# Optimization experiments

Measured on AMD Instinct MI355X. Metric: run time of the kernel, lower is better.

Reference implementation:

```python
import jax, jax.numpy as jnp
import numpy as np

# MoEFeedForward from ViziMarketTransformer (h100_moe_preset dims), eval mode (dropout = identity).
D, F, E, K = 512, 2048, 8, 2   # d_model, d_ff, n_experts, top_k
B, T = 8, 4096
AUX_W = 0.01


def setup_inputs() -> dict:
    key = jax.random.key(0)
    k0, k1, k2, k3 = jax.random.split(key, 4)
    s_in = 1.0 / np.sqrt(D)
    s_mid = 1.0 / np.sqrt(F)
    return {
        "x": jax.random.normal(k0, (B, T, D), jnp.float32),
        "router_w": (jax.random.normal(k1, (D, E), jnp.float32) * s_in),   # nn.Linear(d_model, n_experts, bias=False)
        "w1": (jax.random.normal(k2, (E, D, F), jnp.float32) * s_in),      # per-expert Linear(d_model, d_ff)
        "b1": jnp.zeros((E, F), jnp.float32),
        "w2": (jax.random.normal(k3, (E, F, D), jnp.float32) * s_mid),     # per-expert Linear(d_ff, d_model)
        "b2": jnp.zeros((E, D), jnp.float32),
    }


def reference(x, router_w, w1, b1, w2, b2):
    Bb, Tt, Dd = x.shape
    xf = x.reshape(-1, Dd)                                   # (N, D), N = B*T
    logits = xf @ router_w                                   # (N, E)
    topk_vals, topk_idx = jax.lax.top_k(logits, K)           # (N, K)
    topk_w = jax.nn.softmax(topk_vals, axis=-1)              # (N, K)
    # Combine weights per expert: sum over k of softmax weight where topk_idx == e.
    comb = jnp.sum(jax.nn.one_hot(topk_idx, E, dtype=xf.dtype) * topk_w[..., None], axis=1)  # (N, E)
    out = jnp.zeros_like(xf)
    for e in range(E):  # small fixed expert count; tokens fully vectorized
        h = jax.nn.gelu(xf @ w1[e] + b1[e], approximate=False)   # exact GELU, as nn.GELU()
        out = out + comb[:, e:e + 1] * (h @ w2[e] + b2[e])
    # Switch/GShard auxiliary load-balancing loss.
    probs = jax.nn.softmax(logits, axis=-1)
    avg_prob = probs.mean(axis=0)                             # (E,)
    avg_frac = jax.nn.one_hot(topk_idx[:, 0], E, dtype=xf.dtype).mean(axis=0)  # (E,)
    aux_loss = AUX_W * E * jnp.sum(avg_prob * avg_frac)
    return out.reshape(Bb, Tt, Dd), aux_loss
```

## Files before the change

kernel.cpp:

```cpp
#include <hip/hip_runtime.h>
#include <hip/hip_fp16.h>
#include <cstdint>
#include <cstddef>

#define NTOK 32768
#define DM 512
#define FF 2048
#define NE 8
#define BM 128
#define FBLK 128
#define NFB (FF / FBLK)

typedef _Float16 half8 __attribute__((ext_vector_type(8)));
typedef float floatx4 __attribute__((ext_vector_type(4)));

#define LGKM0_BARRIER() do { \
  asm volatile("s_waitcnt lgkmcnt(0)" ::: "memory"); \
  __builtin_amdgcn_s_barrier(); \
} while (0)

__global__ __launch_bounds__(256) void k_transpose(const float* __restrict__ W,
                                                   _Float16* __restrict__ Wt, int R, int C) {
  __shared__ float tile[32][33];
  int e = blockIdx.z;
  int c0 = blockIdx.x * 32, r0 = blockIdx.y * 32;
  const float* Wp = W + (size_t)e * R * C;
  _Float16* Wtp = Wt + (size_t)e * R * C;
  int tx = threadIdx.x & 31, ty = threadIdx.x >> 5;
  #pragma unroll
  for (int rr = ty; rr < 32; rr += 8)
    tile[rr][tx] = Wp[(size_t)(r0 + rr) * C + c0 + tx];
  __syncthreads();
  #pragma unroll
  for (int cc = ty; cc < 32; cc += 8)
    Wtp[(size_t)(c0 + cc) * R + r0 + tx] = (_Float16)tile[tx][cc];
}

__global__ __launch_bounds__(256) void k_router(
    const float* __restrict__ x, const float* __restrict__ rw,
    _Float16* __restrict__ xb, int* __restrict__ route_e, float* __restrict__ route_w,
    int* __restrict__ counts, float* __restrict__ aux_acc) {
  __shared__ float s_p[NE];
  __shared__ float s_c[NE];
  __shared__ int s_cnt[NE];
  int tid = threadIdx.x, lane = tid & 63, wave = tid >> 6;
  if (tid < NE) { s_p[tid] = 0.f; s_c[tid] = 0.f; s_cnt[tid] = 0; }
  __syncthreads();
  int n = blockIdx.x * 4 + wave;
  const float4* xr = (const float4*)(x + (size_t)n * DM + lane * 8);
  float4 x0 = xr[0], x1 = xr[1];
  float xv[8] = {x0.x, x0.y, x0.z, x0.w, x1.x, x1.y, x1.z, x1.w};
  float acc[NE];
  #pragma unroll
  for (int e = 0; e < NE; e++) acc[e] = 0.f;
  const float4* rwv = (const float4*)rw;
  #pragma unroll
  for (int j = 0; j < 8; j++) {
    int d = lane * 8 + j;
    float4 r0 = rwv[d * 2], r1 = rwv[d * 2 + 1];
    float xd = xv[j];
    acc[0] += xd * r0.x; acc[1] += xd * r0.y; acc[2] += xd * r0.z; acc[3] += xd * r0.w;
    acc[4] += xd * r1.x; acc[5] += xd * r1.y; acc[6] += xd * r1.z; acc[7] += xd * r1.w;
  }
  half8 hv;
  #pragma unroll
  for (int j = 0; j < 8; j++) hv[j] = (_Float16)xv[j];
  *(half8*)(xb + (size_t)n * DM + lane * 8) = hv;
  #pragma unroll
  for (int e = 0; e < NE; e++) {
    #pragma unroll
    for (int m = 1; m < 64; m <<= 1) acc[e] += __shfl_xor(acc[e], m);
  }
  if (lane == 0) {
    int e0 = 0; float v0 = acc[0];
    for (int e = 1; e < NE; e++) if (acc[e] > v0) { v0 = acc[e]; e0 = e; }
    int e1 = (e0 == 0) ? 1 : 0; float v1 = acc[e1];
    for (int e = 0; e < NE; e++) if (e != e0 && acc[e] > v1) { v1 = acc[e]; e1 = e; }
    float w0 = 1.f / (1.f + expf(v1 - v0));
    float w1 = 1.f - w0;
    route_e[n] = e0 | (e1 << 8);
    route_w[2 * n] = w0; route_w[2 * n + 1] = w1;
    float mx = acc[0];
    for (int e = 1; e < NE; e++) mx = fmaxf(mx, acc[e]);
    float p[NE]; float s = 0.f;
    for (int e = 0; e < NE; e++) { p[e] = expf(acc[e] - mx); s += p[e]; }
    float inv = 1.f / s;
    atomicAdd(&s_cnt[e0], 1); atomicAdd(&s_cnt[e1], 1);
    for (int e = 0; e < NE; e++) atomicAdd(&s_p[e], p[e] * inv);
    atomicAdd(&s_c[e0], 1.f);
  }
  __syncthreads();
  if (tid < NE) {
    atomicAdd(&counts[tid], s_cnt[tid]);
    atomicAdd(&aux_acc[tid], s_p[tid]);
    atomicAdd(&aux_acc[NE + tid], s_c[tid]);
  }
}

__global__ void k_finalize(const int* __restrict__ counts, int* __restrict__ offsets,
                           int* __restrict__ cursors, const float* __restrict__ aux_acc,
                           float* __restrict__ out_aux) {
  if (threadIdx.x == 0 && blockIdx.x == 0) {
    int off = 0;
    for (int e = 0; e < NE; e++) { offsets[e] = off; cursors[e] = off; off += counts[e]; }
    const float invN = 1.f / (float)NTOK;
    float aux = 0.f;
    for (int e = 0; e < NE; e++) aux += (aux_acc[e] * invN) * (aux_acc[NE + e] * invN);
    out_aux[0] = 0.01f * (float)NE * aux;
  }
}

__global__ __launch_bounds__(256) void k_build(
    const int* __restrict__ route_e, const float* __restrict__ route_w,
    int* __restrict__ cursors, int* __restrict__ tok, float* __restrict__ wgt,
    int* __restrict__ pos) {
  __shared__ int s_cnt[NE];
  __shared__ int s_base[NE];
  int tid = threadIdx.x;
  if (tid < NE) s_cnt[tid] = 0;
  __syncthreads();
  int n = blockIdx.x * 256 + tid;
  int re = route_e[n];
  int e0 = re & 0xff, e1 = (re >> 8) & 0xff;
  float w0 = route_w[2 * n], w1 = route_w[2 * n + 1];
  int p0 = atomicAdd(&s_cnt[e0], 1);
  int p1 = atomicAdd(&s_cnt[e1], 1);
  __syncthreads();
  if (tid < NE) s_base[tid] = atomicAdd(&cursors[tid], s_cnt[tid]);
  __syncthreads();
  int g0 = s_base[e0] + p0, g1 = s_base[e1] + p1;
  tok[g0] = n; wgt[g0] = w0; pos[n] = g0;
  tok[g1] = n; wgt[g1] = w1; pos[NTOK + n] = g1;
}

__global__ __launch_bounds__(512, 2) void k_fused(
    const _Float16* __restrict__ xb, const _Float16* __restrict__ w1t,
    const _Float16* __restrict__ w2t, const float* __restrict__ b1,
    const float* __restrict__ b2, const int* __restrict__ counts,
    const int* __restrict__ offsets, const int* __restrict__ tok,
    const float* __restrict__ wgt, _Float16* __restrict__ yb) {
  int bid = blockIdx.x;
  int e = bid & 7;
  int tm = bid >> 3;
  int cnt = counts[e];
  if (tm * BM >= cnt) return;
  int off = offsets[e];

  __shared__ _Float16 Xs[2][BM * 32];
  __shared__ _Float16 W1s[2][FBLK * 32];
  __shared__ _Float16 Hs[BM * FBLK];
  __shared__ _Float16 W2s[2][DM * 32];

  int tid = threadIdx.x, lane = tid & 63, wave = tid >> 6;
  int wr = wave >> 2, wc = wave & 3;
  int fr = lane & 15, kfi = lane >> 4;
  int swz = (kfi ^ ((fr >> 1) & 3)) * 8;
  int rowL = tid >> 2, kc = (tid & 3) * 8;
  int stw = rowL * 32 + (((tid & 3) ^ ((tid >> 3) & 3)) * 8);
  int rq = (lane >> 4) * 4, cq = lane & 15;

  int tr = tm * BM + rowL;
  int t0 = tok[off + (tr < cnt ? tr : 0)];
  const _Float16* ax = xb + (size_t)t0 * DM + kc;
  const _Float16* w1e = w1t + (size_t)e * FF * DM;
  const _Float16* w2e = w2t + (size_t)e * DM * FF;
  const _Float16* w2p = w2e + (size_t)rowL * FF + kc;

  floatx4 acc[4][8];
  floatx4 zero = {0.f, 0.f, 0.f, 0.f};
  #pragma unroll
  for (int i = 0; i < 4; i++)
    #pragma unroll
    for (int j = 0; j < 8; j++) acc[i][j] = zero;

  #pragma unroll 1
  for (int fb = 0; fb < NFB; fb++) {
    int fbase = fb * FBLK;
    floatx4 acc1[4][2];
    #pragma unroll
    for (int i = 0; i < 4; i++)
      #pragma unroll
      for (int j = 0; j < 2; j++) acc1[i][j] = zero;
    const _Float16* w1p = w1e + (size_t)(fbase + rowL) * DM + kc;
    half8 ra = *(const half8*)(ax);
    half8 rb = *(const half8*)(w1p);
    *(half8*)(&Xs[0][stw]) = ra;
    *(half8*)(&W1s[0][stw]) = rb;
    ra = *(const half8*)(ax + 32);
    rb = *(const half8*)(w1p + 32);
    LGKM0_BARRIER();
    #pragma unroll
    for (int k = 0; k < 16; k++) {
      int cur = k & 1;
      if (k + 1 < 16) {
        *(half8*)(&Xs[cur ^ 1][stw]) = ra;
        *(half8*)(&W1s[cur ^ 1][stw]) = rb;
      }
      if (k + 2 < 16) {
        ra = *(const half8*)(ax + (k + 2) * 32);
        rb = *(const half8*)(w1p + (k + 2) * 32);
      }
      const _Float16* Ab = &Xs[cur][(wr * 64 + fr) * 32 + swz];
      const _Float16* Bb = &W1s[cur][(wc * 32 + fr) * 32 + swz];
      half8 av[4], bv[2];
      #pragma unroll
      for (int i = 0; i < 4; i++) av[i] = *(const half8*)(Ab + i * 512);
      #pragma unroll
      for (int j = 0; j < 2; j++) bv[j] = *(const half8*)(Bb + j * 512);
      __builtin_amdgcn_s_setprio(1);
      #pragma unroll
      for (int i = 0; i < 4; i++)
        #pragma unroll
        for (int j = 0; j < 2; j++)
          acc1[i][j] = __builtin_amdgcn_mfma_f32_16x16x32_f16(av[i], bv[j], acc1[i][j], 0, 0, 0);
      __builtin_amdgcn_s_setprio(0);
      if (k + 1 < 16) LGKM0_BARRIER();
    }
    #pragma unroll
    for (int j = 0; j < 2; j++) {
      int col = wc * 32 + j * 16 + cq;
      float bb = b1[e * FF + fbase + col];
      #pragma unroll
      for (int i = 0; i < 4; i++) {
        #pragma unroll
        for (int r = 0; r < 4; r++) {
          int row = wr * 64 + i * 16 + rq + r;
          float v = acc1[i][j][r] + bb;
          v = 0.5f * v * (1.f + erff(v * 0.70710678118654752f));
          Hs[row * FBLK + (col ^ ((row & 7) << 3))] = (_Float16)v;
        }
      }
    }
    const _Float16* w2q = w2p + fbase;
    half8 rw0 = *(const half8*)(w2q);
    half8 rw1 = *(const half8*)(w2q + (size_t)128 * FF);
    half8 rw2 = *(const half8*)(w2q + (size_t)256 * FF);
    half8 rw3 = *(const half8*)(w2q + (size_t)384 * FF);
    *(half8*)(&W2s[0][stw]) = rw0;
    *(half8*)(&W2s[0][stw + 128 * 32]) = rw1;
    *(half8*)(&W2s[0][stw + 256 * 32]) = rw2;
    *(half8*)(&W2s[0][stw + 384 * 32]) = rw3;
    rw0 = *(const half8*)(w2q + 32);
    rw1 = *(const half8*)(w2q + (size_t)128 * FF + 32);
    rw2 = *(const half8*)(w2q + (size_t)256 * FF + 32);
    rw3 = *(const half8*)(w2q + (size_t)384 * FF + 32);
    LGKM0_BARRIER();
    #pragma unroll
    for (int k = 0; k < 4; k++) {
      int cur = k & 1;
      if (k + 1 < 4) {
        *(half8*)(&W2s[cur ^ 1][stw]) = rw0;
        *(half8*)(&W2s[cur ^ 1][stw + 128 * 32]) = rw1;
        *(half8*)(&W2s[cur ^ 1][stw + 256 * 32]) = rw2;
        *(half8*)(&W2s[cur ^ 1][stw + 384 * 32]) = rw3;
      }
      if (k + 2 < 4) {
        const _Float16* p = w2q + (k + 2) * 32;
        rw0 = *(const half8*)(p);
        rw1 = *(const half8*)(p + (size_t)128 * FF);
        rw2 = *(const half8*)(p + (size_t)256 * FF);
        rw3 = *(const half8*)(p + (size_t)384 * FF);
      }
      half8 av[4], bv[8];
      #pragma unroll
      for (int i = 0; i < 4; i++) {
        int row = wr * 64 + i * 16 + fr;
        int col = k * 32 + kfi * 8;
        av[i] = *(const half8*)(&Hs[row * FBLK + (col ^ ((row & 7) << 3))]);
      }
      const _Float16* Bb2 = &W2s[cur][(wc * 128 + fr) * 32 + swz];
      #pragma unroll
      for (int j = 0; j < 8; j++)
        bv[j] = *(const half8*)(Bb2 + j * 512);
      __builtin_amdgcn_s_setprio(1);
      #pragma unroll
      for (int i = 0; i < 4; i++)
        #pragma unroll
        for (int j = 0; j < 8; j++)
          acc[i][j] = __builtin_amdgcn_mfma_f32_16x16x32_f16(av[i], bv[j], acc[i][j], 0, 0, 0);
      __builtin_amdgcn_s_setprio(0);
      if (k + 1 < 4) LGKM0_BARRIER();
    }
  }
  float bcol[8];
  #pragma unroll
  for (int j = 0; j < 8; j++) bcol[j] = b2[e * DM + wc * 128 + j * 16 + cq];
  #pragma unroll
  for (int i = 0; i < 4; i++) {
    #pragma unroll
    for (int r = 0; r < 4; r++) {
      int row = tm * BM + wr * 64 + i * 16 + rq + r;
      if (row < cnt) {
        float w = wgt[off + row];
        _Float16* yr = yb + (size_t)(off + row) * DM + wc * 128 + cq;
        #pragma unroll
        for (int j = 0; j < 8; j++)
          yr[j * 16] = (_Float16)(w * (acc[i][j][r] + bcol[j]));
      }
    }
  }
}

__global__ __launch_bounds__(256) void k_combine(
    const _Float16* __restrict__ yb, const int* __restrict__ pos,
    float* __restrict__ out) {
  int tid = threadIdx.x, lane = tid & 63, wave = tid >> 6;
  int n = blockIdx.x * 4 + wave;
  int p0 = pos[n], p1 = pos[NTOK + n];
  half8 a = *(const half8*)(yb + (size_t)p0 * DM + lane * 8);
  half8 b = *(const half8*)(yb + (size_t)p1 * DM + lane * 8);
  float4 o0, o1;
  o0.x = (float)a[0] + (float)b[0];
  o0.y = (float)a[1] + (float)b[1];
  o0.z = (float)a[2] + (float)b[2];
  o0.w = (float)a[3] + (float)b[3];
  o1.x = (float)a[4] + (float)b[4];
  o1.y = (float)a[5] + (float)b[5];
  o1.z = (float)a[6] + (float)b[6];
  o1.w = (float)a[7] + (float)b[7];
  float4* op = (float4*)(out + (size_t)n * DM + lane * 8);
  op[0] = o0; op[1] = o1;
}

extern "C" void kernel_launch(void* const* d_in, const int* in_sizes, int n_in,
                              void* d_out, int out_size, void* d_ws, size_t ws_size,
                              hipStream_t stream) {
  const float* x  = (const float*)d_in[0];
  const float* rw = (const float*)d_in[1];
  const float* w1 = (const float*)d_in[2];
  const float* b1 = (const float*)d_in[3];
  const float* w2 = (const float*)d_in[4];
  const float* b2 = (const float*)d_in[5];
  float* out = (float*)d_out;

  uint8_t* ws = (uint8_t*)d_ws;
  _Float16* xb  = (_Float16*)ws;  ws += (size_t)NTOK * DM * 2;
  _Float16* w1t = (_Float16*)ws;  ws += (size_t)NE * FF * DM * 2;
  _Float16* w2t = (_Float16*)ws;  ws += (size_t)NE * DM * FF * 2;
  int*   tok     = (int*)ws;      ws += (size_t)2 * NTOK * 4;
  float* wgt     = (float*)ws;    ws += (size_t)2 * NTOK * 4;
  int*   pos     = (int*)ws;      ws += (size_t)2 * NTOK * 4;
  int*   route_e = (int*)ws;      ws += (size_t)NTOK * 4;
  float* route_w = (float*)ws;    ws += (size_t)NTOK * 8;
  int*   counts  = (int*)ws;      ws += 8 * 4;
  int*   offsets = (int*)ws;      ws += 8 * 4;
  int*   cursors = (int*)ws;      ws += 8 * 4;
  float* aux     = (float*)ws;    ws += 16 * 4;
  _Float16* yb  = (_Float16*)ws;

  hipMemsetAsync(counts, 0, (8 + 8 + 8 + 16) * 4, stream);

  k_transpose<<<dim3(FF / 32, DM / 32, NE), 256, 0, stream>>>(w1, w1t, DM, FF);
  k_transpose<<<dim3(DM / 32, FF / 32, NE), 256, 0, stream>>>(w2, w2t, FF, DM);
  k_router<<<NTOK / 4, 256, 0, stream>>>(x, rw, xb, route_e, route_w, counts, aux);
  k_finalize<<<1, 64, 0, stream>>>(counts, offsets, cursors, aux, out + (size_t)NTOK * DM);
  k_build<<<NTOK / 256, 256, 0, stream>>>(route_e, route_w, cursors, tok, wgt, pos);
  k_fused<<<(NTOK / BM) * NE, 512, 0, stream>>>(
      xb, w1t, w2t, b1, b2, counts, offsets, tok, wgt, yb);
  k_combine<<<NTOK / 4, 256, 0, stream>>>(yb, pos, out);
}
```

Before: 955.6 us.

## Use direct global-to-LDS loads with triple buffering and register-stream W2

```diff
diff --git a/kernel.cpp b/kernel.cpp
--- a/kernel.cpp
+++ b/kernel.cpp
@@ -10,6 +10,7 @@
 #define BM 128
 #define FBLK 128
 #define NFB (FF / FBLK)
+#define XBUF 4096
 
 typedef _Float16 half8 __attribute__((ext_vector_type(8)));
 typedef float floatx4 __attribute__((ext_vector_type(4)));
@@ -18,6 +19,10 @@
   asm volatile("s_waitcnt lgkmcnt(0)" ::: "memory"); \
   __builtin_amdgcn_s_barrier(); \
 } while (0)
+
+#define GLL16(g, l) __builtin_amdgcn_global_load_lds( \
+    (const __attribute__((address_space(1))) uint32_t*)(g), \
+    (__attribute__((address_space(3))) uint32_t*)(l), 16, 0, 0)
 
 __global__ __launch_bounds__(256) void k_transpose(const float* __restrict__ W,
                                                    _Float16* __restrict__ Wt, int R, int C) {
@@ -146,25 +151,25 @@
   if (tm * BM >= cnt) return;
   int off = offsets[e];
 
-  __shared__ _Float16 Xs[2][BM * 32];
-  __shared__ _Float16 W1s[2][FBLK * 32];
+  __shared__ _Float16 Xs[3][XBUF];
+  __shared__ _Float16 W1s[3][XBUF];
   __shared__ _Float16 Hs[BM * FBLK];
-  __shared__ _Float16 W2s[2][DM * 32];
 
   int tid = threadIdx.x, lane = tid & 63, wave = tid >> 6;
   int wr = wave >> 2, wc = wave & 3;
   int fr = lane & 15, kfi = lane >> 4;
   int swz = (kfi ^ ((fr >> 1) & 3)) * 8;
-  int rowL = tid >> 2, kc = (tid & 3) * 8;
-  int stw = rowL * 32 + (((tid & 3) ^ ((tid >> 3) & 3)) * 8);
+  int rowL = tid >> 2;
+  int kswz = ((tid & 3) ^ ((tid >> 3) & 3)) * 8;
   int rq = (lane >> 4) * 4, cq = lane & 15;
 
   int tr = tm * BM + rowL;
   int t0 = tok[off + (tr < cnt ? tr : 0)];
-  const _Float16* ax = xb + (size_t)t0 * DM + kc;
+  const _Float16* axs = xb + (size_t)t0 * DM + kswz;
   const _Float16* w1e = w1t + (size_t)e * FF * DM;
   const _Float16* w2e = w2t + (size_t)e * DM * FF;
-  const _Float16* w2p = w2e + (size_t)rowL * FF + kc;
+  _Float16* xdst = &Xs[0][0] + wave * 512;
+  _Float16* wdst = &W1s[0][0] + wave * 512;
 
   floatx4 acc[4][8];
   floatx4 zero = {0.f, 0.f, 0.f, 0.f};
@@ -181,25 +186,22 @@
     for (int i = 0; i < 4; i++)
       #pragma unroll
       for (int j = 0; j < 2; j++) acc1[i][j] = zero;
-    const _Float16* w1p = w1e + (size_t)(fbase + rowL) * DM + kc;
-    half8 ra = *(const half8*)(ax);
-    half8 rb = *(const half8*)(w1p);
-    *(half8*)(&Xs[0][stw]) = ra;
-    *(half8*)(&W1s[0][stw]) = rb;
-    ra = *(const half8*)(ax + 32);
-    rb = *(const half8*)(w1p + 32);
-    LGKM0_BARRIER();
+    const _Float16* w1ps = w1e + (size_t)(fbase + rowL) * DM + kswz;
+    GLL16(axs, xdst);
+    GLL16(w1ps, wdst);
+    GLL16(axs + 32, xdst + XBUF);
+    GLL16(w1ps + 32, wdst + XBUF);
     #pragma unroll
     for (int k = 0; k < 16; k++) {
-      int cur = k & 1;
-      if (k + 1 < 16) {
-        *(half8*)(&Xs[cur ^ 1][stw]) = ra;
-        *(half8*)(&W1s[cur ^ 1][stw]) = rb;
-      }
+      if (k < 15) { asm volatile("s_waitcnt vmcnt(2)" ::: "memory"); }
+      else       { asm volatile("s_waitcnt vmcnt(0)" ::: "memory"); }
+      __builtin_amdgcn_s_barrier();
       if (k + 2 < 16) {
-        ra = *(const half8*)(ax + (k + 2) * 32);
-        rb = *(const half8*)(w1p + (k + 2) * 32);
-      }
+        int nb = (k + 2) % 3;
+        GLL16(axs + (k + 2) * 32, xdst + nb * XBUF);
+        GLL16(w1ps + (k + 2) * 32, wdst + nb * XBUF);
+      }
+      int cur = k % 3;
       const _Float16* Ab = &Xs[cur][(wr * 64 + fr) * 32 + swz];
       const _Float16* Bb = &W1s[cur][(wc * 32 + fr) * 32 + swz];
       half8 av[4], bv[2];
@@ -214,7 +216,7 @@
         for (int j = 0; j < 2; j++)
           acc1[i][j] = __builtin_amdgcn_mfma_f32_16x16x32_f16(av[i], bv[j], acc1[i][j], 0, 0, 0);
       __builtin_amdgcn_s_setprio(0);
-      if (k + 1 < 16) LGKM0_BARRIER();
+      asm volatile("s_waitcnt lgkmcnt(0)" ::: "memory");
     }
     #pragma unroll
     for (int j = 0; j < 2; j++) {
@@ -231,55 +233,32 @@
         }
       }
     }
-    const _Float16* w2q = w2p + fbase;
-    half8 rw0 = *(const half8*)(w2q);
-    half8 rw1 = *(const half8*)(w2q + (size_t)128 * FF);
-    half8 rw2 = *(const half8*)(w2q + (size_t)256 * FF);
-    half8 rw3 = *(const half8*)(w2q + (size_t)384 * FF);
-    *(half8*)(&W2s[0][stw]) = rw0;
-    *(half8*)(&W2s[0][stw + 128 * 32]) = rw1;
-    *(half8*)(&W2s[0][stw + 256 * 32]) = rw2;
-    *(half8*)(&W2s[0][stw + 384 * 32]) = rw3;
-    rw0 = *(const half8*)(w2q + 32);
-    rw1 = *(const half8*)(w2q + (size_t)128 * FF + 32);
-    rw2 = *(const half8*)(w2q + (size_t)256 * FF + 32);
-    rw3 = *(const half8*)(w2q + (size_t)384 * FF + 32);
     LGKM0_BARRIER();
-    #pragma unroll
-    for (int k = 0; k < 4; k++) {
-      int cur = k & 1;
-      if (k + 1 < 4) {
-        *(half8*)(&W2s[cur ^ 1][stw]) = rw0;
-        *(half8*)(&W2s[cur ^ 1][stw + 128 * 32]) = rw1;
-        *(half8*)(&W2s[cur ^ 1][stw + 256 * 32]) = rw2;
-        *(half8*)(&W2s[cur ^ 1][stw + 384 * 32]) = rw3;
-      }
-      if (k + 2 < 4) {
-        const _Float16* p = w2q + (k + 2) * 32;
-        rw0 = *(const half8*)(p);
-        rw1 = *(const half8*)(p + (size_t)128 * FF);
-        rw2 = *(const half8*)(p + (size_t)256 * FF);
-        rw3 = *(const half8*)(p + (size_t)384 * FF);
-      }
-      half8 av[4], bv[8];
+    const _Float16* w2c = w2e + (size_t)(wc * 128 + fr) * FF + fbase + kfi * 8;
+    half8 bq[2][8];
+    #pragma unroll
+    for (int j = 0; j < 8; j++) bq[0][j] = *(const half8*)(w2c + (size_t)j * 16 * FF);
+    #pragma unroll
+    for (int kk = 0; kk < 4; kk++) {
+      if (kk + 1 < 4) {
+        #pragma unroll
+        for (int j = 0; j < 8; j++)
+          bq[(kk + 1) & 1][j] = *(const half8*)(w2c + (size_t)j * 16 * FF + (kk + 1) * 32);
+      }
+      half8 av2[4];
       #pragma unroll
       for (int i = 0; i < 4; i++) {
         int row = wr * 64 + i * 16 + fr;
-        int col = k * 32 + kfi * 8;
-        av[i] = *(const half8*)(&Hs[row * FBLK + (col ^ ((row & 7) << 3))]);
-      }
-      const _Float16* Bb2 = &W2s[cur][(wc * 128 + fr) * 32 + swz];
-      #pragma unroll
-      for (int j = 0; j < 8; j++)
-        bv[j] = *(const half8*)(Bb2 + j * 512);
+        int col = kk * 32 + kfi * 8;
+        av2[i] = *(const half8*)(&Hs[row * FBLK + (col ^ ((row & 7) << 3))]);
+      }
       __builtin_amdgcn_s_setprio(1);
       #pragma unroll
       for (int i = 0; i < 4; i++)
         #pragma unroll
         for (int j = 0; j < 8; j++)
-          acc[i][j] = __builtin_amdgcn_mfma_f32_16x16x32_f16(av[i], bv[j], acc[i][j], 0, 0, 0);
+          acc[i][j] = __builtin_amdgcn_mfma_f32_16x16x32_f16(av2[i], bq[kk & 1][j], acc[i][j], 0, 0, 0);
       __builtin_amdgcn_s_setprio(0);
-      if (k + 1 < 4) LGKM0_BARRIER();
     }
   }
   float bcol[8];
```

After: 1.543 ms. 1.61x slower.
